# Kernel optimization log

Measured on AMD Instinct MI355X. Metric: run time of the kernel, lower is better.

## Reference

```python
import jax, jax.numpy as jnp
import numpy as np

SIGMA = 1.0
NUM_LAYERS = 1
B, N, D, CD = 4, 256, 128, 3


def setup_inputs() -> dict:
    key = jax.random.key(0)
    ks = jax.random.split(key, 10)
    s = lambda fan_in: 1.0 / np.sqrt(fan_in)
    return {
        "local_emb": jax.random.normal(ks[0], (B, N, D), dtype=jnp.float32),
        "coords": jax.random.normal(ks[1], (B, N, CD), dtype=jnp.float32),
        # msg_mlp: Linear(2D -> D), ReLU, Linear(D -> D). Weights stored [in, out].
        "mW1": jax.random.uniform(ks[2], (2 * D, D), jnp.float32, -s(2 * D), s(2 * D)),
        "mb1": jax.random.uniform(ks[3], (D,), jnp.float32, -s(2 * D), s(2 * D)),
        "mW2": jax.random.uniform(ks[4], (D, D), jnp.float32, -s(D), s(D)),
        "mb2": jax.random.uniform(ks[5], (D,), jnp.float32, -s(D), s(D)),
        # update_mlp: Linear(D+CD -> D), ReLU, Linear(D -> D)
        "uW1": jax.random.uniform(ks[6], (D + CD, D), jnp.float32, -s(D + CD), s(D + CD)),
        "ub1": jax.random.uniform(ks[7], (D,), jnp.float32, -s(D + CD), s(D + CD)),
        "uW2": jax.random.uniform(ks[8], (D, D), jnp.float32, -s(D), s(D)),
        "ub2": jax.random.uniform(ks[9], (D,), jnp.float32, -s(D), s(D)),
    }


def reference(local_emb, coords, mW1, mb1, mW2, mb2, uW1, ub1, uW2, ub2):
    # Split msg_mlp first layer: Linear(concat([h_i, h_j])) == h_i @ W1a + h_j @ W1b
    W1a, W1b = mW1[:D], mW1[D:]
    for _ in range(NUM_LAYERS):
        # Gaussian affinity A[b,i,j] = exp(-||c_i - c_j||^2 / (2 sigma^2))
        diff = coords[:, :, None, :] - coords[:, None, :, :]        # [B,N,N,CD]
        dist2 = jnp.sum(diff * diff, axis=-1)                        # [B,N,N]
        A = jnp.exp(-dist2 / (2.0 * SIGMA ** 2))
        # Pairwise message MLP: pre[b,i,j,:] = h_i W1a + h_j W1b + b1
        pre = (jnp.einsum("bid,de->bie", local_emb, W1a)[:, :, None, :]
               + jnp.einsum("bjd,de->bje", local_emb, W1b)[:, None, :, :]
               + mb1)                                                # [B,N,N,D]
        msgs = jnp.einsum("bijd,de->bije", jax.nn.relu(pre), mW2) + mb2
        # Gaussian-weighted aggregation
        agg = jnp.einsum("bij,bijd->bid", A, msgs)                   # [B,N,D]
        # Update MLP on [agg, coords]
        upd_in = jnp.concatenate([agg, coords], axis=-1)             # [B,N,D+CD]
        delta = jax.nn.relu(upd_in @ uW1 + ub1) @ uW2 + ub2
        local_emb = local_emb + delta
    return local_emb
```

## Files before the change

### kernel.cpp

```cpp
#include <hip/hip_runtime.h>
#include <math.h>

#define NN 256
#define DD 128

typedef float4 f4;

#define FMA4(acc, s, v)                          \
  acc.x = fmaf(s, v.x, acc.x);                   \
  acc.y = fmaf(s, v.y, acc.y);                   \
  acc.z = fmaf(s, v.z, acc.z);                   \
  acc.w = fmaf(s, v.w, acc.w);

#define FMA4R(acc, a, p, v)                              \
  acc.x = fmaf(a, fmaxf(p.x + v.x, 0.f), acc.x);         \
  acc.y = fmaf(a, fmaxf(p.y + v.y, 0.f), acc.y);         \
  acc.z = fmaf(a, fmaxf(p.z + v.z, 0.f), acc.z);         \
  acc.w = fmaf(a, fmaxf(p.w + v.w, 0.f), acc.w);

#define ZERO4 {0.f, 0.f, 0.f, 0.f}

__device__ __forceinline__ void stage_128k(const float* __restrict__ g,
                                           float* l, int tid) {
    const int wave = tid >> 6, lane = tid & 63;
    #pragma unroll
    for (int k = 0; k < 16; ++k) {
        const int chunk = wave * 16 + k;
        __builtin_amdgcn_global_load_lds(
            (__attribute__((address_space(1))) void*)(void*)(g + chunk * 256 + lane * 4),
            (__attribute__((address_space(3))) void*)(l + chunk * 256),
            16, 0, 0);
    }
}

__global__ __launch_bounds__(512, 2) void h1_kernel(
    const float* __restrict__ emb,
    const float* __restrict__ mW1,
    const float* __restrict__ mb1,
    float* __restrict__ H1a,
    float* __restrict__ H1b)
{
    const int tid  = threadIdx.x;
    const int row0 = blockIdx.x * 4;

    __shared__ float WL[32768];
    __shared__ f4 embT[DD];

    const int rs = tid >> 7, ks = tid & 127;
    const float ev = emb[(size_t)(row0 + rs) * DD + ks];
    stage_128k(mW1, WL, tid);
    ((float*)embT)[ks * 4 + rs] = ev;
    __syncthreads();

    const int oq  = tid & 63;
    const int kh  = tid >> 6;
    const int wq  = oq & 31;
    const int wr0 = (oq < 32) ? 0 : DD;
    const f4* __restrict__ WL4 = (const f4*)WL;

    f4 a0 = ZERO4, a1 = ZERO4, a2 = ZERO4, a3 = ZERO4;
    #pragma unroll
    for (int t = 0; t < 16; ++t) {
        const int k = kh * 16 + t;
        const f4 w  = WL4[(wr0 + k) * 32 + wq];
        const f4 e4 = embT[k];
        FMA4(a0, e4.x, w);
        FMA4(a1, e4.y, w);
        FMA4(a2, e4.z, w);
        FMA4(a3, e4.w, w);
    }
    __syncthreads();

    f4* red4 = (f4*)WL;
    red4[(kh * 4 + 0) * 64 + oq] = a0;
    red4[(kh * 4 + 1) * 64 + oq] = a1;
    red4[(kh * 4 + 2) * 64 + oq] = a2;
    red4[(kh * 4 + 3) * 64 + oq] = a3;
    __syncthreads();

    const float* __restrict__ redF = (const float*)WL;
    #pragma unroll
    for (int t = 0; t < 2; ++t) {
        const int o  = t * 512 + tid;
        const int rr = o >> 8, oc = o & 255;
        float v = 0.f;
        #pragma unroll
        for (int q = 0; q < 8; ++q) v += redF[(q * 4 + rr) * 256 + oc];
        if (oc < DD) H1a[(size_t)(row0 + rr) * DD + oc]        = v + mb1[oc];
        else         H1b[(size_t)(row0 + rr) * DD + (oc - DD)] = v;
    }
}

__global__ __launch_bounds__(512, 2) void gnn_kernel(
    const float* __restrict__ emb,
    const float* __restrict__ coords,
    const float* __restrict__ mW2, const float* __restrict__ mb2,
    const float* __restrict__ uW1, const float* __restrict__ ub1,
    const float* __restrict__ uW2, const float* __restrict__ ub2,
    const float* __restrict__ H1a, const float* __restrict__ H1b,
    float* __restrict__ out)
{
    const int tid  = threadIdx.x;
    const int row0 = blockIdx.x * 4;
    const int b    = row0 >> 8;
    const int i0   = row0 & 255;

    __shared__ float HbL[32768];
    __shared__ float cS[NN * 3];
    __shared__ f4 As4[NN];
    __shared__ f4 R_T[DD];
    __shared__ f4 U_T[DD + 3];
    __shared__ f4 h_T[DD];
    __shared__ f4 sAs4[16];
    __shared__ float sAtot[4];

    const int eq = tid & 31;
    const int js = tid >> 5;

    const f4* __restrict__ Ha4 = (const f4*)(H1a + (size_t)row0 * DD);
    const f4 pa0 = Ha4[0 * 32 + eq];
    const f4 pa1 = Ha4[1 * 32 + eq];
    const f4 pa2 = Ha4[2 * 32 + eq];
    const f4 pa3 = Ha4[3 * 32 + eq];
    const int rr2 = tid >> 7, ea = tid & 127;
    const float embv = emb[(size_t)(row0 + rr2) * DD + ea];
    const float mb2v = mb2[ea], ub1v = ub1[ea], ub2v = ub2[ea];
    const float* __restrict__ cb = coords + (size_t)b * NN * 3;
    f4 cldv = ZERO4;
    if (tid < 192) cldv = ((const f4*)cb)[tid];

    stage_128k(H1b + (size_t)b * NN * DD, HbL, tid);
    if (tid < 192) ((f4*)cS)[tid] = cldv;
    __syncthreads();

    {   const int j = tid & 255, rA = tid >> 8;
        const float cjx = cS[j * 3], cjy = cS[j * 3 + 1], cjz = cS[j * 3 + 2];
        float* __restrict__ AsF = (float*)As4;
        {   const int ii = i0 + rA;
            const float dx = cjx - cS[ii * 3], dy = cjy - cS[ii * 3 + 1], dz = cjz - cS[ii * 3 + 2];
            AsF[j * 4 + rA] = __expf(-0.5f * (dx * dx + dy * dy + dz * dz)); }
        {   const int ii = i0 + rA + 2;
            const float dx = cjx - cS[ii * 3], dy = cjy - cS[ii * 3 + 1], dz = cjz - cS[ii * 3 + 2];
            AsF[j * 4 + rA + 2] = __expf(-0.5f * (dx * dx + dy * dy + dz * dz)); }
    }
    __syncthreads();

    const f4* __restrict__ Hb4 = (const f4*)HbL;
    f4 a0 = ZERO4, a1 = ZERO4, a2 = ZERO4, a3 = ZERO4, sA4 = ZERO4;
    #pragma unroll
    for (int t = 0; t < 16; ++t) {
        const int j = js * 16 + t;
        const f4 a = As4[j];
        const f4 v = Hb4[j * 32 + eq];
        sA4.x += a.x; sA4.y += a.y; sA4.z += a.z; sA4.w += a.w;
        FMA4R(a0, a.x, pa0, v);
        FMA4R(a1, a.y, pa1, v);
        FMA4R(a2, a.z, pa2, v);
        FMA4R(a3, a.w, pa3, v);
    }
    __syncthreads();

    f4* red4 = (f4*)HbL;
    red4[(js * 4 + 0) * 32 + eq] = a0;
    red4[(js * 4 + 1) * 32 + eq] = a1;
    red4[(js * 4 + 2) * 32 + eq] = a2;
    red4[(js * 4 + 3) * 32 + eq] = a3;
    if (eq == 0) sAs4[js] = sA4;
    const int kh = js, cq = eq;
    f4 wv[8];
    {   const f4* __restrict__ W2g = (const f4*)mW2;
        #pragma unroll
        for (int t = 0; t < 8; ++t) wv[t] = W2g[(size_t)(kh * 8 + t) * 32 + cq];
    }
    __syncthreads();

    const float* __restrict__ redF = (const float*)HbL;
    {   const int r = tid >> 7, e = tid & 127;
        float s = 0.f;
        #pragma unroll
        for (int q = 0; q < 16; ++q) s += redF[(q * 4 + r) * 128 + e];
        ((float*)R_T)[e * 4 + r] = s;
    }
    if (tid < 4) {
        const float* __restrict__ sF = (const float*)sAs4;
        float s = 0.f;
        #pragma unroll
        for (int q = 0; q < 16; ++q) s += sF[q * 4 + tid];
        sAtot[tid] = s;
    }
    __syncthreads();

    {   f4 g0 = ZERO4, g1 = ZERO4, g2 = ZERO4, g3 = ZERO4;
        #pragma unroll
        for (int t = 0; t < 8; ++t) {
            const f4 rv = R_T[kh * 8 + t];
            FMA4(g0, rv.x, wv[t]);
            FMA4(g1, rv.y, wv[t]);
            FMA4(g2, rv.z, wv[t]);
            FMA4(g3, rv.w, wv[t]);
        }
        red4[(kh * 4 + 0) * 32 + cq] = g0;
        red4[(kh * 4 + 1) * 32 + cq] = g1;
        red4[(kh * 4 + 2) * 32 + cq] = g2;
        red4[(kh * 4 + 3) * 32 + cq] = g3;
    }
    f4 wt0 = ZERO4, wt1 = ZERO4, wt2 = ZERO4;
    {   const f4* __restrict__ U1g = (const f4*)uW1;
        #pragma unroll
        for (int t = 0; t < 8; ++t) wv[t] = U1g[(size_t)(kh * 8 + t) * 32 + cq];
        if (kh == 15) {
            wt0 = U1g[(size_t)(DD + 0) * 32 + cq];
            wt1 = U1g[(size_t)(DD + 1) * 32 + cq];
            wt2 = U1g[(size_t)(DD + 2) * 32 + cq];
        }
    }
    __syncthreads();

    {   const int r = tid >> 7, e = tid & 127;
        float s = sAtot[r] * mb2v;
        #pragma unroll
        for (int q = 0; q < 16; ++q) s += redF[(q * 4 + r) * 128 + e];
        ((float*)U_T)[e * 4 + r] = s;
    }
    if (tid < 12) {
        const int r = tid & 3, c = tid >> 2;
        ((float*)U_T)[(DD + c) * 4 + r] = cS[(i0 + r) * 3 + c];
    }
    __syncthreads();

    {   f4 g0 = ZERO4, g1 = ZERO4, g2 = ZERO4, g3 = ZERO4;
        #pragma unroll
        for (int t = 0; t < 8; ++t) {
            const f4 uv = U_T[kh * 8 + t];
            FMA4(g0, uv.x, wv[t]);
            FMA4(g1, uv.y, wv[t]);
            FMA4(g2, uv.z, wv[t]);
            FMA4(g3, uv.w, wv[t]);
        }
        if (kh == 15) {
            const f4 uv0 = U_T[DD + 0], uv1 = U_T[DD + 1], uv2 = U_T[DD + 2];
            FMA4(g0, uv0.x, wt0); FMA4(g1, uv0.y, wt0); FMA4(g2, uv0.z, wt0); FMA4(g3, uv0.w, wt0);
            FMA4(g0, uv1.x, wt1); FMA4(g1, uv1.y, wt1); FMA4(g2, uv1.z, wt1); FMA4(g3, uv1.w, wt1);
            FMA4(g0, uv2.x, wt2); FMA4(g1, uv2.y, wt2); FMA4(g2, uv2.z, wt2); FMA4(g3, uv2.w, wt2);
        }
        red4[(kh * 4 + 0) * 32 + cq] = g0;
        red4[(kh * 4 + 1) * 32 + cq] = g1;
        red4[(kh * 4 + 2) * 32 + cq] = g2;
        red4[(kh * 4 + 3) * 32 + cq] = g3;
    }
    {   const f4* __restrict__ U2g = (const f4*)uW2;
        #pragma unroll
        for (int t = 0; t < 8; ++t) wv[t] = U2g[(size_t)(kh * 8 + t) * 32 + cq];
    }
    __syncthreads();

    {   const int r = tid >> 7, e = tid & 127;
        float s = ub1v;
        #pragma unroll
        for (int q = 0; q < 16; ++q) s += redF[(q * 4 + r) * 128 + e];
        ((float*)h_T)[e * 4 + r] = fmaxf(s, 0.f);
    }
    __syncthreads();

    {   f4 g0 = ZERO4, g1 = ZERO4, g2 = ZERO4, g3 = ZERO4;
        #pragma unroll
        for (int t = 0; t < 8; ++t) {
            const f4 hv = h_T[kh * 8 + t];
            FMA4(g0, hv.x, wv[t]);
            FMA4(g1, hv.y, wv[t]);
            FMA4(g2, hv.z, wv[t]);
            FMA4(g3, hv.w, wv[t]);
        }
        red4[(kh * 4 + 0) * 32 + cq] = g0;
        red4[(kh * 4 + 1) * 32 + cq] = g1;
        red4[(kh * 4 + 2) * 32 + cq] = g2;
        red4[(kh * 4 + 3) * 32 + cq] = g3;
    }
    __syncthreads();

    {   const int r = tid >> 7, e = tid & 127;
        float s = ub2v;
        #pragma unroll
        for (int q = 0; q < 16; ++q) s += redF[(q * 4 + r) * 128 + e];
        out[(size_t)(row0 + r) * DD + e] = embv + s;
    }
}

extern "C" void kernel_launch(void* const* d_in, const int* in_sizes, int n_in,
                              void* d_out, int out_size, void* d_ws, size_t ws_size,
                              hipStream_t stream) {
    const float* emb    = (const float*)d_in[0];
    const float* coords = (const float*)d_in[1];
    const float* mW1    = (const float*)d_in[2];
    const float* mb1    = (const float*)d_in[3];
    const float* mW2    = (const float*)d_in[4];
    const float* mb2    = (const float*)d_in[5];
    const float* uW1    = (const float*)d_in[6];
    const float* ub1    = (const float*)d_in[7];
    const float* uW2    = (const float*)d_in[8];
    const float* ub2    = (const float*)d_in[9];
    float* out = (float*)d_out;

    float* H1a = (float*)d_ws;
    float* H1b = H1a + 4 * NN * DD;

    h1_kernel<<<dim3(256), dim3(512), 0, stream>>>(emb, mW1, mb1, H1a, H1b);
    gnn_kernel<<<dim3(256), dim3(512), 0, stream>>>(
        emb, coords, mW2, mb2, uW1, ub1, uW2, ub2, H1a, H1b, out);
}
```

Before: 86.55 us.

## Fuse H1 projection into GNN kernel, recomputing per-batch H1b in each block

Merges the two launches into one kernel, where each block computes its own H1a rows and recomputes the full per-batch H1b projection in LDS using a register-tiled 8x16 outer product. This removes the intermediate global write/read and one kernel launch. In exchange, every block redundantly recomputes the entire batch's H1b, adding substantial extra FLOPs, and runs with 256 threads and one block per CU.

```diff
diff --git a/kernel.cpp b/kernel.cpp
--- a/kernel.cpp
+++ b/kernel.cpp
@@ -20,84 +20,16 @@
 
 #define ZERO4 {0.f, 0.f, 0.f, 0.f}
 
-__device__ __forceinline__ void stage_128k(const float* __restrict__ g,
-                                           float* l, int tid) {
-    const int wave = tid >> 6, lane = tid & 63;
-    #pragma unroll
-    for (int k = 0; k < 16; ++k) {
-        const int chunk = wave * 16 + k;
-        __builtin_amdgcn_global_load_lds(
-            (__attribute__((address_space(1))) void*)(void*)(g + chunk * 256 + lane * 4),
-            (__attribute__((address_space(3))) void*)(l + chunk * 256),
-            16, 0, 0);
-    }
-}
-
-__global__ __launch_bounds__(512, 2) void h1_kernel(
-    const float* __restrict__ emb,
-    const float* __restrict__ mW1,
-    const float* __restrict__ mb1,
-    float* __restrict__ H1a,
-    float* __restrict__ H1b)
-{
-    const int tid  = threadIdx.x;
-    const int row0 = blockIdx.x * 4;
-
-    __shared__ float WL[32768];
-    __shared__ f4 embT[DD];
-
-    const int rs = tid >> 7, ks = tid & 127;
-    const float ev = emb[(size_t)(row0 + rs) * DD + ks];
-    stage_128k(mW1, WL, tid);
-    ((float*)embT)[ks * 4 + rs] = ev;
-    __syncthreads();
-
-    const int oq  = tid & 63;
-    const int kh  = tid >> 6;
-    const int wq  = oq & 31;
-    const int wr0 = (oq < 32) ? 0 : DD;
-    const f4* __restrict__ WL4 = (const f4*)WL;
-
-    f4 a0 = ZERO4, a1 = ZERO4, a2 = ZERO4, a3 = ZERO4;
-    #pragma unroll
-    for (int t = 0; t < 16; ++t) {
-        const int k = kh * 16 + t;
-        const f4 w  = WL4[(wr0 + k) * 32 + wq];
-        const f4 e4 = embT[k];
-        FMA4(a0, e4.x, w);
-        FMA4(a1, e4.y, w);
-        FMA4(a2, e4.z, w);
-        FMA4(a3, e4.w, w);
-    }
-    __syncthreads();
-
-    f4* red4 = (f4*)WL;
-    red4[(kh * 4 + 0) * 64 + oq] = a0;
-    red4[(kh * 4 + 1) * 64 + oq] = a1;
-    red4[(kh * 4 + 2) * 64 + oq] = a2;
-    red4[(kh * 4 + 3) * 64 + oq] = a3;
-    __syncthreads();
-
-    const float* __restrict__ redF = (const float*)WL;
-    #pragma unroll
-    for (int t = 0; t < 2; ++t) {
-        const int o  = t * 512 + tid;
-        const int rr = o >> 8, oc = o & 255;
-        float v = 0.f;
-        #pragma unroll
-        for (int q = 0; q < 8; ++q) v += redF[(q * 4 + rr) * 256 + oc];
-        if (oc < DD) H1a[(size_t)(row0 + rr) * DD + oc]        = v + mb1[oc];
-        else         H1b[(size_t)(row0 + rr) * DD + (oc - DD)] = v;
-    }
-}
-
-__global__ __launch_bounds__(512, 2) void gnn_kernel(
+#define AS1 __attribute__((address_space(1)))
+#define AS3 __attribute__((address_space(3)))
+
+__global__ __launch_bounds__(256, 1) void fused_gnn(
     const float* __restrict__ emb,
     const float* __restrict__ coords,
+    const float* __restrict__ mW1, const float* __restrict__ mb1,
     const float* __restrict__ mW2, const float* __restrict__ mb2,
     const float* __restrict__ uW1, const float* __restrict__ ub1,
     const float* __restrict__ uW2, const float* __restrict__ ub2,
-    const float* __restrict__ H1a, const float* __restrict__ H1b,
     float* __restrict__ out)
 {
     const int tid  = threadIdx.x;
@@ -105,121 +37,257 @@
     const int b    = row0 >> 8;
     const int i0   = row0 & 255;
 
-    __shared__ float HbL[32768];
+    __shared__ float BIG[32768];
     __shared__ float cS[NN * 3];
     __shared__ f4 As4[NN];
+    __shared__ float paS[4 * DD];
     __shared__ f4 R_T[DD];
     __shared__ f4 U_T[DD + 3];
     __shared__ f4 h_T[DD];
-    __shared__ f4 sAs4[16];
+    __shared__ f4 sAs4[8];
     __shared__ float sAtot[4];
+
+    float* embT  = BIG;
+    float* W1bC0 = BIG + 16384;
+    float* W1bC1 = BIG + 24576;
+
+    const f4* __restrict__ emb4 = (const f4*)emb;
+    const f4* __restrict__ mW14 = (const f4*)mW1;
+
+    if (tid < 192) ((f4*)cS)[tid] = ((const f4*)(coords + (size_t)b * NN * 3))[tid];
+
+    const int a_ = tid >> 4, b_ = tid & 15;
+    f4 ev[16];
+    #pragma unroll
+    for (int i = 0; i < 16; ++i)
+        ev[i] = emb4[(size_t)(b * NN + (b_ + 16 * i)) * 32 + a_];
+
+    {
+        const float* g0 = mW1 + (size_t)(DD + 0) * DD;
+        const float* g1 = mW1 + (size_t)(DD + 64) * DD;
+        const int wave = tid >> 6, lane = tid & 63;
+        #pragma unroll
+        for (int k = 0; k < 8; ++k) {
+            const int c = wave * 8 + k;
+            __builtin_amdgcn_global_load_lds((AS1 void*)(void*)(g0 + c * 256 + lane * 4),
+                                             (AS3 void*)(W1bC0 + c * 256), 16, 0, 0);
+        }
+        #pragma unroll
+        for (int k = 0; k < 8; ++k) {
+            const int c = wave * 8 + k;
+            __builtin_amdgcn_global_load_lds((AS1 void*)(void*)(g1 + c * 256 + lane * 4),
+                                             (AS3 void*)(W1bC1 + c * 256), 16, 0, 0);
+        }
+    }
+
+    #pragma unroll
+    for (int i = 0; i < 16; ++i) {
+        const int row = b_ + 16 * i;
+        embT[(4 * a_ + 0) * 256 + row] = ev[i].x;
+        embT[(4 * a_ + 1) * 256 + row] = ev[i].y;
+        embT[(4 * a_ + 2) * 256 + row] = ev[i].z;
+        embT[(4 * a_ + 3) * 256 + row] = ev[i].w;
+    }
+    __syncthreads();
+
+    if (tid < 128) {
+        const int rr = tid >> 5, cq = tid & 31;
+        f4 acc = ZERO4;
+        const f4* __restrict__ erow = emb4 + (size_t)(row0 + rr) * 32;
+        #pragma unroll 8
+        for (int kq = 0; kq < 32; ++kq) {
+            const f4 e  = erow[kq];
+            const f4 w0 = mW14[(size_t)(4 * kq + 0) * 32 + cq];
+            const f4 w1 = mW14[(size_t)(4 * kq + 1) * 32 + cq];
+            const f4 w2 = mW14[(size_t)(4 * kq + 2) * 32 + cq];
+            const f4 w3 = mW14[(size_t)(4 * kq + 3) * 32 + cq];
+            FMA4(acc, e.x, w0);
+            FMA4(acc, e.y, w1);
+            FMA4(acc, e.z, w2);
+            FMA4(acc, e.w, w3);
+        }
+        const f4 mb = ((const f4*)mb1)[cq];
+        acc.x += mb.x; acc.y += mb.y; acc.z += mb.z; acc.w += mb.w;
+        ((f4*)paS)[rr * 32 + cq] = acc;
+    } else {
+        const int t2 = tid - 128;
+        #pragma unroll
+        for (int u = 0; u < 2; ++u) {
+            const int jj = 2 * t2 + u;
+            const float cjx = cS[jj * 3], cjy = cS[jj * 3 + 1], cjz = cS[jj * 3 + 2];
+            f4 av;
+            float* avF = (float*)&av;
+            #pragma unroll
+            for (int r = 0; r < 4; ++r) {
+                const int ii = i0 + r;
+                const float dx = cjx - cS[ii * 3], dy = cjy - cS[ii * 3 + 1], dz = cjz - cS[ii * 3 + 2];
+                avF[r] = __expf(-0.5f * (dx * dx + dy * dy + dz * dz));
+            }
+            As4[jj] = av;
+        }
+    }
+
+    f4 ev1[16];
+    #pragma unroll
+    for (int i = 0; i < 16; ++i)
+        ev1[i] = emb4[(size_t)(b * NN + (b_ + 16 * i)) * 32 + 16 + a_];
+
+    const int rg = tid >> 3, cg = tid & 7;
+    f4 acc[8][4];
+    #pragma unroll
+    for (int r = 0; r < 8; ++r)
+        #pragma unroll
+        for (int q = 0; q < 4; ++q) acc[r][q] = (f4)ZERO4;
+
+    const f4* __restrict__ Wb0 = (const f4*)W1bC0;
+    #pragma unroll 4
+    for (int kl = 0; kl < 64; ++kl) {
+        const f4 e0 = *(const f4*)&embT[kl * 256 + 8 * rg];
+        const f4 e1 = *(const f4*)&embT[kl * 256 + 8 * rg + 4];
+        f4 w[4];
+        #pragma unroll
+        for (int q = 0; q < 4; ++q) w[q] = Wb0[kl * 32 + cg + 8 * q];
+        #pragma unroll
+        for (int q = 0; q < 4; ++q) {
+            FMA4(acc[0][q], e0.x, w[q]);
+            FMA4(acc[1][q], e0.y, w[q]);
+            FMA4(acc[2][q], e0.z, w[q]);
+            FMA4(acc[3][q], e0.w, w[q]);
+            FMA4(acc[4][q], e1.x, w[q]);
+            FMA4(acc[5][q], e1.y, w[q]);
+            FMA4(acc[6][q], e1.z, w[q]);
+            FMA4(acc[7][q], e1.w, w[q]);
+        }
+    }
+    __syncthreads();
+
+    #pragma unroll
+    for (int i = 0; i < 16; ++i) {
+        const int row = b_ + 16 * i;
+        embT[(4 * a_ + 0) * 256 + row] = ev1[i].x;
+        embT[(4 * a_ + 1) * 256 + row] = ev1[i].y;
+        embT[(4 * a_ + 2) * 256 + row] = ev1[i].z;
+        embT[(4 * a_ + 3) * 256 + row] = ev1[i].w;
+    }
+    __syncthreads();
+
+    const f4* __restrict__ Wb1 = (const f4*)W1bC1;
+    #pragma unroll 4
+    for (int kl = 0; kl < 64; ++kl) {
+        const f4 e0 = *(const f4*)&embT[kl * 256 + 8 * rg];
+        const f4 e1 = *(const f4*)&embT[kl * 256 + 8 * rg + 4];
+        f4 w[4];
+        #pragma unroll
+        for (int q = 0; q < 4; ++q) w[q] = Wb1[kl * 32 + cg + 8 * q];
+        #pragma unroll
+        for (int q = 0; q < 4; ++q) {
+            FMA4(acc[0][q], e0.x, w[q]);
+            FMA4(acc[1][q], e0.y, w[q]);
+            FMA4(acc[2][q], e0.z, w[q]);
+            FMA4(acc[3][q], e0.w, w[q]);
+            FMA4(acc[4][q], e1.x, w[q]);
+            FMA4(acc[5][q], e1.y, w[q]);
+            FMA4(acc[6][q], e1.z, w[q]);
+            FMA4(acc[7][q], e1.w, w[q]);
+        }
+    }
+    __syncthreads();
+
+    f4* H1b4 = (f4*)BIG;
+    #pragma unroll
+    for (int r = 0; r < 8; ++r)
+        #pragma unroll
+        for (int q = 0; q < 4; ++q)
+            H1b4[(8 * rg + r) * 32 + cg + 8 * q] = acc[r][q];
+    __syncthreads();
 
     const int eq = tid & 31;
     const int js = tid >> 5;
 
-    const f4* __restrict__ Ha4 = (const f4*)(H1a + (size_t)row0 * DD);
-    const f4 pa0 = Ha4[0 * 32 + eq];
-    const f4 pa1 = Ha4[1 * 32 + eq];
-    const f4 pa2 = Ha4[2 * 32 + eq];
-    const f4 pa3 = Ha4[3 * 32 + eq];
-    const int rr2 = tid >> 7, ea = tid & 127;
-    const float embv = emb[(size_t)(row0 + rr2) * DD + ea];
-    const float mb2v = mb2[ea], ub1v = ub1[ea], ub2v = ub2[ea];
-    const float* __restrict__ cb = coords + (size_t)b * NN * 3;
-    f4 cldv = ZERO4;
-    if (tid < 192) cldv = ((const f4*)cb)[tid];
-
-    stage_128k(H1b + (size_t)b * NN * DD, HbL, tid);
-    if (tid < 192) ((f4*)cS)[tid] = cldv;
-    __syncthreads();
-
-    {   const int j = tid & 255, rA = tid >> 8;
-        const float cjx = cS[j * 3], cjy = cS[j * 3 + 1], cjz = cS[j * 3 + 2];
-        float* __restrict__ AsF = (float*)As4;
-        {   const int ii = i0 + rA;
-            const float dx = cjx - cS[ii * 3], dy = cjy - cS[ii * 3 + 1], dz = cjz - cS[ii * 3 + 2];
-            AsF[j * 4 + rA] = __expf(-0.5f * (dx * dx + dy * dy + dz * dz)); }
-        {   const int ii = i0 + rA + 2;
-            const float dx = cjx - cS[ii * 3], dy = cjy - cS[ii * 3 + 1], dz = cjz - cS[ii * 3 + 2];
-            AsF[j * 4 + rA + 2] = __expf(-0.5f * (dx * dx + dy * dy + dz * dz)); }
-    }
-    __syncthreads();
-
-    const f4* __restrict__ Hb4 = (const f4*)HbL;
-    f4 a0 = ZERO4, a1 = ZERO4, a2 = ZERO4, a3 = ZERO4, sA4 = ZERO4;
-    #pragma unroll
-    for (int t = 0; t < 16; ++t) {
-        const int j = js * 16 + t;
+    const f4 pa0 = ((const f4*)paS)[0 * 32 + eq];
+    const f4 pa1 = ((const f4*)paS)[1 * 32 + eq];
+    const f4 pa2 = ((const f4*)paS)[2 * 32 + eq];
+    const f4 pa3 = ((const f4*)paS)[3 * 32 + eq];
+
+    f4 j0 = ZERO4, j1 = ZERO4, j2 = ZERO4, j3 = ZERO4, sA4 = ZERO4;
+    #pragma unroll 8
+    for (int t = 0; t < 32; ++t) {
+        const int j = js * 32 + t;
         const f4 a = As4[j];
-        const f4 v = Hb4[j * 32 + eq];
+        const f4 v = H1b4[j * 32 + eq];
         sA4.x += a.x; sA4.y += a.y; sA4.z += a.z; sA4.w += a.w;
-        FMA4R(a0, a.x, pa0, v);
-        FMA4R(a1, a.y, pa1, v);
-        FMA4R(a2, a.z, pa2, v);
-        FMA4R(a3, a.w, pa3, v);
-    }
-    __syncthreads();
-
-    f4* red4 = (f4*)HbL;
-    red4[(js * 4 + 0) * 32 + eq] = a0;
-    red4[(js * 4 + 1) * 32 + eq] = a1;
-    red4[(js * 4 + 2) * 32 + eq] = a2;
-    red4[(js * 4 + 3) * 32 + eq] = a3;
+        FMA4R(j0, a.x, pa0, v);
+        FMA4R(j1, a.y, pa1, v);
+        FMA4R(j2, a.z, pa2, v);
+        FMA4R(j3, a.w, pa3, v);
+    }
+    __syncthreads();
+
+    f4* red4 = (f4*)BIG;
+    red4[(js * 4 + 0) * 32 + eq] = j0;
+    red4[(js * 4 + 1) * 32 + eq] = j1;
+    red4[(js * 4 + 2) * 32 + eq] = j2;
+    red4[(js * 4 + 3) * 32 + eq] = j3;
     if (eq == 0) sAs4[js] = sA4;
-    const int kh = js, cq = eq;
-    f4 wv[8];
+    f4 wv[16];
     {   const f4* __restrict__ W2g = (const f4*)mW2;
         #pragma unroll
-        for (int t = 0; t < 8; ++t) wv[t] = W2g[(size_t)(kh * 8 + t) * 32 + cq];
-    }
-    __syncthreads();
-
-    const float* __restrict__ redF = (const float*)HbL;
-    {   const int r = tid >> 7, e = tid & 127;
+        for (int t = 0; t < 16; ++t) wv[t] = W2g[(size_t)(js * 16 + t) * 32 + eq];
+    }
+    __syncthreads();
+
+    const float* __restrict__ redF = (const float*)BIG;
+    #pragma unroll
+    for (int tt = 0; tt < 2; ++tt) {
+        const int o = tt * 256 + tid;
+        const int r = o >> 7, e = o & 127;
         float s = 0.f;
         #pragma unroll
-        for (int q = 0; q < 16; ++q) s += redF[(q * 4 + r) * 128 + e];
+        for (int q = 0; q < 8; ++q) s += redF[(q * 4 + r) * 128 + e];
         ((float*)R_T)[e * 4 + r] = s;
     }
     if (tid < 4) {
         const float* __restrict__ sF = (const float*)sAs4;
         float s = 0.f;
         #pragma unroll
-        for (int q = 0; q < 16; ++q) s += sF[q * 4 + tid];
+        for (int q = 0; q < 8; ++q) s += sF[q * 4 + tid];
         sAtot[tid] = s;
     }
     __syncthreads();
 
     {   f4 g0 = ZERO4, g1 = ZERO4, g2 = ZERO4, g3 = ZERO4;
         #pragma unroll
-        for (int t = 0; t < 8; ++t) {
-            const f4 rv = R_T[kh * 8 + t];
+        for (int t = 0; t < 16; ++t) {
+            const f4 rv = R_T[js * 16 + t];
             FMA4(g0, rv.x, wv[t]);
             FMA4(g1, rv.y, wv[t]);
             FMA4(g2, rv.z, wv[t]);
             FMA4(g3, rv.w, wv[t]);
         }
-        red4[(kh * 4 + 0) * 32 + cq] = g0;
-        red4[(kh * 4 + 1) * 32 + cq] = g1;
-        red4[(kh * 4 + 2) * 32 + cq] = g2;
-        red4[(kh * 4 + 3) * 32 + cq] = g3;
+        red4[(js * 4 + 0) * 32 + eq] = g0;
+        red4[(js * 4 + 1) * 32 + eq] = g1;
+        red4[(js * 4 + 2) * 32 + eq] = g2;
+        red4[(js * 4 + 3) * 32 + eq] = g3;
     }
     f4 wt0 = ZERO4, wt1 = ZERO4, wt2 = ZERO4;
     {   const f4* __restrict__ U1g = (const f4*)uW1;
         #pragma unroll
-        for (int t = 0; t < 8; ++t) wv[t] = U1g[(size_t)(kh * 8 + t) * 32 + cq];
-        if (kh == 15) {
-            wt0 = U1g[(size_t)(DD + 0) * 32 + cq];
-            wt1 = U1g[(size_t)(DD + 1) * 32 + cq];
-            wt2 = U1g[(size_t)(DD + 2) * 32 + cq];
-        }
-    }
-    __syncthreads();
-
-    {   const int r = tid >> 7, e = tid & 127;
-        float s = sAtot[r] * mb2v;
-        #pragma unroll
-        for (int q = 0; q < 16; ++q) s += redF[(q * 4 + r) * 128 + e];
+        for (int t = 0; t < 16; ++t) wv[t] = U1g[(size_t)(js * 16 + t) * 32 + eq];
+        if (js == 7) {
+            wt0 = U1g[(size_t)(DD + 0) * 32 + eq];
+            wt1 = U1g[(size_t)(DD + 1) * 32 + eq];
+            wt2 = U1g[(size_t)(DD + 2) * 32 + eq];
+        }
+    }
+    __syncthreads();
+
+    #pragma unroll
+    for (int tt = 0; tt < 2; ++tt) {
+        const int o = tt * 256 + tid;
+        const int r = o >> 7, e = o & 127;
+        float s = sAtot[r] * mb2[e];
+        #pragma unroll
+        for (int q = 0; q < 8; ++q) s += redF[(q * 4 + r) * 128 + e];
         ((float*)U_T)[e * 4 + r] = s;
     }
     if (tid < 12) {
@@ -230,59 +298,65 @@
 
     {   f4 g0 = ZERO4, g1 = ZERO4, g2 = ZERO4, g3 = ZERO4;
         #pragma unroll
-        for (int t = 0; t < 8; ++t) {
-            const f4 uv = U_T[kh * 8 + t];
+        for (int t = 0; t < 16; ++t) {
+            const f4 uv = U_T[js * 16 + t];
             FMA4(g0, uv.x, wv[t]);
             FMA4(g1, uv.y, wv[t]);
             FMA4(g2, uv.z, wv[t]);
             FMA4(g3, uv.w, wv[t]);
         }
-        if (kh == 15) {
+        if (js == 7) {
             const f4 uv0 = U_T[DD + 0], uv1 = U_T[DD + 1], uv2 = U_T[DD + 2];
             FMA4(g0, uv0.x, wt0); FMA4(g1, uv0.y, wt0); FMA4(g2, uv0.z, wt0); FMA4(g3, uv0.w, wt0);
             FMA4(g0, uv1.x, wt1); FMA4(g1, uv1.y, wt1); FMA4(g2, uv1.z, wt1); FMA4(g3, uv1.w, wt1);
             FMA4(g0, uv2.x, wt2); FMA4(g1, uv2.y, wt2); FMA4(g2, uv2.z, wt2); FMA4(g3, uv2.w, wt2);
         }
-        red4[(kh * 4 + 0) * 32 + cq] = g0;
-        red4[(kh * 4 + 1) * 32 + cq] = g1;
-        red4[(kh * 4 + 2) * 32 + cq] = g2;
-        red4[(kh * 4 + 3) * 32 + cq] = g3;
+        red4[(js * 4 + 0) * 32 + eq] = g0;
+        red4[(js * 4 + 1) * 32 + eq] = g1;
+        red4[(js * 4 + 2) * 32 + eq] = g2;
+        red4[(js * 4 + 3) * 32 + eq] = g3;
     }
     {   const f4* __restrict__ U2g = (const f4*)uW2;
         #pragma unroll
-        for (int t = 0; t < 8; ++t) wv[t] = U2g[(size_t)(kh * 8 + t) * 32 + cq];
-    }
-    __syncthreads();
-
-    {   const int r = tid >> 7, e = tid & 127;
-        float s = ub1v;
-        #pragma unroll
-        for (int q = 0; q < 16; ++q) s += redF[(q * 4 + r) * 128 + e];
+        for (int t = 0; t < 16; ++t) wv[t] = U2g[(size_t)(js * 16 + t) * 32 + eq];
+    }
+    __syncthreads();
+
+    #pragma unroll
+    for (int tt = 0; tt < 2; ++tt) {
+        const int o = tt * 256 + tid;
+        const int r = o >> 7, e = o & 127;
+        float s = ub1[e];
+        #pragma unroll
+        for (int q = 0; q < 8; ++q) s += redF[(q * 4 + r) * 128 + e];
         ((float*)h_T)[e * 4 + r] = fmaxf(s, 0.f);
     }
     __syncthreads();
 
     {   f4 g0 = ZERO4, g1 = ZERO4, g2 = ZERO4, g3 = ZERO4;
         #pragma unroll
-        for (int t = 0; t < 8; ++t) {
-            const f4 hv = h_T[kh * 8 + t];
+        for (int t = 0; t < 16; ++t) {
+            const f4 hv = h_T[js * 16 + t];
             FMA4(g0, hv.x, wv[t]);
             FMA4(g1, hv.y, wv[t]);
             FMA4(g2, hv.z, wv[t]);
             FMA4(g3, hv.w, wv[t]);
         }
-        red4[(kh * 4 + 0) * 32 + cq] = g0;
-        red4[(kh * 4 + 1) * 32 + cq] = g1;
-        red4[(kh * 4 + 2) * 32 + cq] = g2;
-        red4[(kh * 4 + 3) * 32 + cq] = g3;
-    }
-    __syncthreads();
-
-    {   const int r = tid >> 7, e = tid & 127;
-        float s = ub2v;
-        #pragma unroll
-        for (int q = 0; q < 16; ++q) s += redF[(q * 4 + r) * 128 + e];
-        out[(size_t)(row0 + r) * DD + e] = embv + s;
+        red4[(js * 4 + 0) * 32 + eq] = g0;
+        red4[(js * 4 + 1) * 32 + eq] = g1;
+        red4[(js * 4 + 2) * 32 + eq] = g2;
+        red4[(js * 4 + 3) * 32 + eq] = g3;
+    }
+    __syncthreads();
+
+    #pragma unroll
+    for (int tt = 0; tt < 2; ++tt) {
+        const int o = tt * 256 + tid;
+        const int r = o >> 7, e = o & 127;
+        float s = ub2[e];
+        #pragma unroll
+        for (int q = 0; q < 8; ++q) s += redF[(q * 4 + r) * 128 + e];
+        out[(size_t)(row0 + r) * DD + e] = emb[(size_t)(row0 + r) * DD + e] + s;
     }
 }
 
@@ -301,10 +375,6 @@
     const float* ub2    = (const float*)d_in[9];
     float* out = (float*)d_out;
 
-    float* H1a = (float*)d_ws;
-    float* H1b = H1a + 4 * NN * DD;
-
-    h1_kernel<<<dim3(256), dim3(512), 0, stream>>>(emb, mW1, mb1, H1a, H1b);
-    gnn_kernel<<<dim3(256), dim3(512), 0, stream>>>(
-        emb, coords, mW2, mb2, uW1, ub1, uW2, ub2, H1a, H1b, out);
+    fused_gnn<<<dim3(256), dim3(256), 0, stream>>>(
+        emb, coords, mW1, mb1, mW2, mb2, uW1, ub1, uW2, ub2, out);
 }
```

Result: slower. 108.4 us (+25.2%).
